# Kernel tuning notes

Measured on AMD Instinct MI355X. Metric: run time of the kernel, lower is better.

The kernel has to match this reference:

```python
import jax, jax.numpy as jnp
import numpy as np

D = 2048      # hidden
H = 16        # heads
HD = 128      # head dim
E = 64        # experts
K = 8         # top-k
F = 1024      # expert intermediate
B, S = 1, 256
EPS = 1e-05
THETA = 10000.0
SCALE = 0.08838834764831845  # 1/sqrt(128)


def _rms(x, w):
    return x * jax.lax.rsqrt(jnp.mean(x * x, axis=-1, keepdims=True) + EPS) * w


def _rotate_half(x):
    h = x.shape[-1] // 2
    return jnp.concatenate([-x[..., h:], x[..., :h]], axis=-1)


def setup_inputs() -> dict:
    key = jax.random.key(0)
    ks = jax.random.split(key, 16)
    std = 0.02
    return {
        "x": jax.random.normal(ks[0], (B, S, D), jnp.float32),
        "ln1_w": jnp.ones((D,), jnp.float32),
        "q_w": jax.random.normal(ks[1], (D, D), jnp.float32) * std,
        "k_w": jax.random.normal(ks[2], (D, D), jnp.float32) * std,
        "v_w": jax.random.normal(ks[3], (D, D), jnp.float32) * std,
        "o_w": jax.random.normal(ks[4], (D, D), jnp.float32) * std,
        "qn_w": jnp.ones((D,), jnp.float32),
        "kn_w": jnp.ones((D,), jnp.float32),
        "ln2_w": jnp.ones((D,), jnp.float32),
        "router_w": jax.random.normal(ks[5], (E, D), jnp.float32) * std,
        "gate_w": jax.random.normal(ks[6], (E, F, D), jnp.float32) * std,
        "up_w": jax.random.normal(ks[7], (E, F, D), jnp.float32) * std,
        "down_w": jax.random.normal(ks[8], (E, D, F), jnp.float32) * std,
    }


def reference(x, ln1_w, q_w, k_w, v_w, o_w, qn_w, kn_w, ln2_w,
              router_w, gate_w, up_w, down_w):
    b, s, d = x.shape
    # ---- attention ----
    xn = _rms(x, ln1_w)
    q = _rms(jnp.einsum('bsd,od->bso', xn, q_w), qn_w)
    k = _rms(jnp.einsum('bsd,od->bso', xn, k_w), kn_w)
    v = jnp.einsum('bsd,od->bso', xn, v_w)
    q = q.reshape(b, s, H, HD).transpose(0, 2, 1, 3)  # [b,h,s,hd]
    k = k.reshape(b, s, H, HD).transpose(0, 2, 1, 3)
    v = v.reshape(b, s, H, HD).transpose(0, 2, 1, 3)
    # RoPE
    inv_freq = 1.0 / (THETA ** (jnp.arange(0, HD, 2, dtype=jnp.float32) / HD))
    ang = jnp.arange(s, dtype=jnp.float32)[:, None] * inv_freq[None, :]  # [s, hd/2]
    emb = jnp.concatenate([ang, ang], axis=-1)
    cos, sin = jnp.cos(emb).astype(x.dtype), jnp.sin(emb).astype(x.dtype)
    q = q * cos + _rotate_half(q) * sin
    k = k * cos + _rotate_half(k) * sin
    scores = jnp.einsum('bhqd,bhkd->bhqk', q, k) * SCALE
    causal = jnp.tril(jnp.ones((s, s), bool))
    scores = jnp.where(causal, scores, jnp.finfo(scores.dtype).min)
    attn = jax.nn.softmax(scores, axis=-1)
    ctx = jnp.einsum('bhqk,bhkd->bhqd', attn, v)
    ctx = ctx.transpose(0, 2, 1, 3).reshape(b, s, d)
    h = x + jnp.einsum('bsd,od->bso', ctx, o_w)
    # ---- MoE ----
    hn = _rms(h, ln2_w)
    logits = jnp.einsum('bsd,ed->bse', hn, router_w)
    probs = jax.nn.softmax(logits.astype(jnp.float32), axis=-1)
    vals, idx = jax.lax.top_k(probs, K)  # [b,s,K]
    # dense combine weights [b,s,E]; OLMoE does not renormalize top-k probs
    combine = jnp.sum(jax.nn.one_hot(idx, E, dtype=jnp.float32) * vals[..., None], axis=-2)
    combine = combine.reshape(-1, E).astype(x.dtype)  # [T,E]
    xf = hn.reshape(-1, d)                            # [T,D]
    g = jnp.einsum('td,efd->etf', xf, gate_w)         # [E,T,F]
    u = jnp.einsum('td,efd->etf', xf, up_w)
    mid = jax.nn.silu(g) * u
    eo = jnp.einsum('etf,edf->etd', mid, down_w)      # [E,T,D]
    y = jnp.einsum('te,etd->td', combine, eo).reshape(b, s, d)
    return h + y
```

## Files before the change

### kernel.cpp

```cpp
#include <hip/hip_runtime.h>
#include <math.h>

#define DHID 2048
#define TOK 256
#define NHEAD 16
#define HDIM 128
#define NEXP 64
#define KSEL 8
#define FFD 1024
#define RMSEPS 1e-5f
#define ATTNSCALE 0.08838834764831845f

typedef short bf16x8 __attribute__((ext_vector_type(8)));
typedef float f32x4 __attribute__((ext_vector_type(4)));

__device__ __forceinline__ float bf2f(unsigned short u){
  union { unsigned int u; float f; } c; c.u = ((unsigned int)u)<<16; return c.f;
}
__device__ __forceinline__ unsigned short f2bf(float f){
  union { float f; unsigned int u; } c; c.f = f;
  unsigned int u = c.u + 0x7fffu + ((c.u>>16)&1u);
  return (unsigned short)(u>>16);
}
__device__ __forceinline__ unsigned int pk2(float a, float b){
  return (unsigned int)f2bf(a) | ((unsigned int)f2bf(b)<<16);
}

__global__ __launch_bounds__(256) void rms_kernel(const float* __restrict__ x,
    const float* __restrict__ w, unsigned short* __restrict__ obf,
    float* __restrict__ of32)
{
  int row = blockIdx.x, tid = threadIdx.x;
  const float* xr = x + (size_t)row*DHID;
  float4 a = *(const float4*)(xr + tid*8);
  float4 b = *(const float4*)(xr + tid*8 + 4);
  float ss = a.x*a.x+a.y*a.y+a.z*a.z+a.w*a.w + b.x*b.x+b.y*b.y+b.z*b.z+b.w*b.w;
  #pragma unroll
  for(int o=32;o>0;o>>=1) ss += __shfl_down(ss,o);
  __shared__ float red[4];
  if((tid&63)==0) red[tid>>6]=ss;
  __syncthreads();
  float r = rsqrtf((red[0]+red[1]+red[2]+red[3])*(1.0f/DHID) + RMSEPS);
  float v[8] = {a.x,a.y,a.z,a.w,b.x,b.y,b.z,b.w};
  unsigned short ob[8];
  #pragma unroll
  for(int j=0;j<8;j++){
    float val = v[j]*r*w[tid*8+j];
    ob[j]=f2bf(val);
    if(of32) of32[(size_t)row*DHID + tid*8 + j] = val;
  }
  uint4 o4;
  o4.x = (unsigned int)ob[0] | ((unsigned int)ob[1]<<16);
  o4.y = (unsigned int)ob[2] | ((unsigned int)ob[3]<<16);
  o4.z = (unsigned int)ob[4] | ((unsigned int)ob[5]<<16);
  o4.w = (unsigned int)ob[6] | ((unsigned int)ob[7]<<16);
  *(uint4*)(obf + (size_t)row*DHID + tid*8) = o4;
}

__global__ void rope_table_kernel(float* __restrict__ cs, float* __restrict__ sn){
  int i = blockIdx.x*256 + threadIdx.x;
  int s = i>>6, j = i&63;
  float invf = powf(10000.0f, -(float)j*(1.0f/64.0f));
  float ang = (float)s * invf;
  cs[i] = cosf(ang); sn[i] = sinf(ang);
}

__global__ __launch_bounds__(256) void gemm_qkv_kernel(
    const unsigned short* __restrict__ A,
    const float* __restrict__ qw, const float* __restrict__ kw, const float* __restrict__ vw,
    float* __restrict__ qo, float* __restrict__ ko, float* __restrict__ vo)
{
  int nt = blockIdx.x, mt = blockIdx.y;
  int which = nt>>5, nb = nt&31;
  const float* W = (which==0)? qw : (which==1)? kw : vw;
  float* OUT = (which==0)? qo : (which==1)? ko : vo;
  int n0 = nb*64, m0 = mt*64;
  __shared__ unsigned short As[64*64];
  __shared__ unsigned short Bs[64*64];
  int tid = threadIdx.x;
  int wid = tid>>6, lane = tid&63;
  int wm = wid>>1, wn = wid&1;
  int lr = lane&15, lg = lane>>4;
  int sr = tid>>2, sq = tid&3;
  f32x4 acc[2][2] = {};
  const unsigned short* Ap = A + (size_t)(m0+sr)*DHID + sq*16;
  const float* Bp = W + (size_t)(n0+sr)*DHID + sq*16;
  for(int k0=0;k0<DHID;k0+=64){
    uint4 a0 = *(const uint4*)(Ap + k0);
    uint4 a1 = *(const uint4*)(Ap + k0 + 8);
    float4 b0 = *(const float4*)(Bp + k0);
    float4 b1 = *(const float4*)(Bp + k0 + 4);
    float4 b2 = *(const float4*)(Bp + k0 + 8);
    float4 b3 = *(const float4*)(Bp + k0 + 12);
    int x7 = sr&7;
    *(uint4*)&As[sr*64 + (((sq*2)  ^ x7)*8)] = a0;
    *(uint4*)&As[sr*64 + (((sq*2+1)^ x7)*8)] = a1;
    uint4 p0 = make_uint4(pk2(b0.x,b0.y),pk2(b0.z,b0.w),pk2(b1.x,b1.y),pk2(b1.z,b1.w));
    uint4 p1 = make_uint4(pk2(b2.x,b2.y),pk2(b2.z,b2.w),pk2(b3.x,b3.y),pk2(b3.z,b3.w));
    *(uint4*)&Bs[sr*64 + (((sq*2)  ^ x7)*8)] = p0;
    *(uint4*)&Bs[sr*64 + (((sq*2+1)^ x7)*8)] = p1;
    __syncthreads();
    #pragma unroll
    for(int ki=0;ki<2;ki++){
      bf16x8 af[2], bfr[2];
      #pragma unroll
      for(int mi=0;mi<2;mi++){
        int r = wm*32 + mi*16 + lr;
        af[mi] = *(const bf16x8*)&As[r*64 + (((ki*4+lg)^(r&7))*8)];
      }
      #pragma unroll
      for(int ni=0;ni<2;ni++){
        int r = wn*32 + ni*16 + lr;
        bfr[ni] = *(const bf16x8*)&Bs[r*64 + (((ki*4+lg)^(r&7))*8)];
      }
      #pragma unroll
      for(int mi=0;mi<2;mi++)
        #pragma unroll
        for(int ni=0;ni<2;ni++)
          acc[mi][ni] = __builtin_amdgcn_mfma_f32_16x16x32_bf16(af[mi], bfr[ni], acc[mi][ni], 0,0,0);
    }
    __syncthreads();
  }
  #pragma unroll
  for(int mi=0;mi<2;mi++){
    #pragma unroll
    for(int ni=0;ni<2;ni++){
      int col = n0 + wn*32 + ni*16 + lr;
      int rowb = m0 + wm*32 + mi*16 + lg*4;
      #pragma unroll
      for(int rg=0;rg<4;rg++)
        OUT[(size_t)(rowb+rg)*DHID + col] = acc[mi][ni][rg];
    }
  }
}

__global__ __launch_bounds__(256) void gemm_o_kernel(const float* __restrict__ A,
  const float* __restrict__ W, const float* __restrict__ X,
  float* __restrict__ H, float* __restrict__ O)
{
  int nb = blockIdx.x, mt = blockIdx.y;
  int n0 = nb*64, m0 = mt*64;
  __shared__ unsigned short As[64*64];
  __shared__ unsigned short Bs[64*64];
  int tid = threadIdx.x;
  int wid = tid>>6, lane = tid&63;
  int wm = wid>>1, wn = wid&1;
  int lr = lane&15, lg = lane>>4;
  int sr = tid>>2, sq = tid&3;
  f32x4 acc[2][2] = {};
  const float* Ap = A + (size_t)(m0+sr)*DHID + sq*16;
  const float* Bp = W + (size_t)(n0+sr)*DHID + sq*16;
  for(int k0=0;k0<DHID;k0+=64){
    float4 a0=*(const float4*)(Ap+k0),   a1=*(const float4*)(Ap+k0+4);
    float4 a2=*(const float4*)(Ap+k0+8), a3=*(const float4*)(Ap+k0+12);
    float4 b0=*(const float4*)(Bp+k0),   b1=*(const float4*)(Bp+k0+4);
    float4 b2=*(const float4*)(Bp+k0+8), b3=*(const float4*)(Bp+k0+12);
    int x7 = sr&7;
    uint4 pa0 = make_uint4(pk2(a0.x,a0.y),pk2(a0.z,a0.w),pk2(a1.x,a1.y),pk2(a1.z,a1.w));
    uint4 pa1 = make_uint4(pk2(a2.x,a2.y),pk2(a2.z,a2.w),pk2(a3.x,a3.y),pk2(a3.z,a3.w));
    uint4 pb0 = make_uint4(pk2(b0.x,b0.y),pk2(b0.z,b0.w),pk2(b1.x,b1.y),pk2(b1.z,b1.w));
    uint4 pb1 = make_uint4(pk2(b2.x,b2.y),pk2(b2.z,b2.w),pk2(b3.x,b3.y),pk2(b3.z,b3.w));
    *(uint4*)&As[sr*64 + (((sq*2)  ^ x7)*8)] = pa0;
    *(uint4*)&As[sr*64 + (((sq*2+1)^ x7)*8)] = pa1;
    *(uint4*)&Bs[sr*64 + (((sq*2)  ^ x7)*8)] = pb0;
    *(uint4*)&Bs[sr*64 + (((sq*2+1)^ x7)*8)] = pb1;
    __syncthreads();
    #pragma unroll
    for(int ki=0;ki<2;ki++){
      bf16x8 af[2], bfr[2];
      #pragma unroll
      for(int mi=0;mi<2;mi++){
        int r = wm*32 + mi*16 + lr;
        af[mi] = *(const bf16x8*)&As[r*64 + (((ki*4+lg)^(r&7))*8)];
      }
      #pragma unroll
      for(int ni=0;ni<2;ni++){
        int r = wn*32 + ni*16 + lr;
        bfr[ni] = *(const bf16x8*)&Bs[r*64 + (((ki*4+lg)^(r&7))*8)];
      }
      #pragma unroll
      for(int mi=0;mi<2;mi++)
        #pragma unroll
        for(int ni=0;ni<2;ni++)
          acc[mi][ni] = __builtin_amdgcn_mfma_f32_16x16x32_bf16(af[mi], bfr[ni], acc[mi][ni], 0,0,0);
    }
    __syncthreads();
  }
  #pragma unroll
  for(int mi=0;mi<2;mi++){
    #pragma unroll
    for(int ni=0;ni<2;ni++){
      int col = n0 + wn*32 + ni*16 + lr;
      int rowb = m0 + wm*32 + mi*16 + lg*4;
      #pragma unroll
      for(int rg=0;rg<4;rg++){
        size_t idx = (size_t)(rowb+rg)*DHID + col;
        float v = acc[mi][ni][rg] + X[idx];
        H[idx] = v; O[idx] = v;
      }
    }
  }
}

__global__ __launch_bounds__(256) void qknorm_rope_kernel(const float* __restrict__ in,
   const float* __restrict__ w, const float* __restrict__ cs, const float* __restrict__ sn,
   float* __restrict__ out)
{
  int t = blockIdx.x, tid = threadIdx.x;
  __shared__ float xs[DHID];
  const float* xr = in + (size_t)t*DHID;
  float4 a = *(const float4*)(xr + tid*8);
  float4 b = *(const float4*)(xr + tid*8 + 4);
  *(float4*)&xs[tid*8] = a; *(float4*)&xs[tid*8+4] = b;
  float ss = a.x*a.x+a.y*a.y+a.z*a.z+a.w*a.w + b.x*b.x+b.y*b.y+b.z*b.z+b.w*b.w;
  #pragma unroll
  for(int o=32;o>0;o>>=1) ss += __shfl_down(ss,o);
  __shared__ float red[4];
  if((tid&63)==0) red[tid>>6]=ss;
  __syncthreads();
  float r = rsqrtf((red[0]+red[1]+red[2]+red[3])*(1.0f/DHID) + RMSEPS);
  int hh = tid>>4, jb = (tid&15)*4;
  #pragma unroll
  for(int p=0;p<4;p++){
    int j = jb+p;
    int i0 = hh*HDIM + j, i1 = i0+64;
    float va = xs[i0]*r*w[i0];
    float vb = xs[i1]*r*w[i1];
    float c = cs[t*64+j], s = sn[t*64+j];
    out[((size_t)(hh*TOK + t))*HDIM + j]    = va*c - vb*s;
    out[((size_t)(hh*TOK + t))*HDIM + j+64] = vb*c + va*s;
  }
}

__global__ __launch_bounds__(256) void vreshape_kernel(const float* __restrict__ v,
    float* __restrict__ vh)
{
  int t = blockIdx.x, tid = threadIdx.x;
  int i = tid*8;
  int hh = i>>7, d0 = i&127;
  float4 a = *(const float4*)(v + (size_t)t*DHID + i);
  float4 b = *(const float4*)(v + (size_t)t*DHID + i + 4);
  *(float4*)(vh + ((size_t)(hh*TOK+t))*HDIM + d0)     = a;
  *(float4*)(vh + ((size_t)(hh*TOK+t))*HDIM + d0 + 4) = b;
}

__global__ __launch_bounds__(256) void attn_kernel(const float* __restrict__ qh,
  const float* __restrict__ kh, const float* __restrict__ vh, float* __restrict__ ctx)
{
  int head = blockIdx.x>>4, qt = blockIdx.x&15;
  __shared__ float qs[16][132];
  __shared__ float sc[16][260];
  __shared__ float red[16][16];
  __shared__ float rmx[16], rsm[16];
  int tid = threadIdx.x;
  {
    int r = tid>>4, c = (tid&15)*8;
    const float* src = qh + ((size_t)(head*TOK + qt*16 + r))*HDIM + c;
    *(float4*)&qs[r][c]   = *(const float4*)(src);
    *(float4*)&qs[r][c+4] = *(const float4*)(src+4);
  }
  __syncthreads();
  int qi = tid&15, kk = tid>>4;
  int qg = qt*16 + qi;
  for(int k=kk; k<=qg; k+=16){
    const float* kp = kh + ((size_t)(head*TOK + k))*HDIM;
    float d = 0.f;
    #pragma unroll 8
    for(int c=0;c<128;c+=4){
      float4 kv = *(const float4*)(kp + c);
      float4 qv = *(const float4*)&qs[qi][c];
      d += qv.x*kv.x + qv.y*kv.y + qv.z*kv.z + qv.w*kv.w;
    }
    sc[qi][k] = d*ATTNSCALE;
  }
  float m = -1e30f;
  for(int k=kk;k<=qg;k+=16) m = fmaxf(m, sc[qi][k]);
  red[qi][kk] = m;
  __syncthreads();
  if(kk==0){
    float mm=-1e30f;
    #pragma unroll
    for(int j=0;j<16;j++) mm = fmaxf(mm, red[qi][j]);
    rmx[qi]=mm;
  }
  __syncthreads();
  float mm = rmx[qi];
  float s = 0.f;
  for(int k=kk;k<=qg;k+=16){ float pp = expf(sc[qi][k]-mm); sc[qi][k]=pp; s+=pp; }
  red[qi][kk]=s;
  __syncthreads();
  if(kk==0){
    float t_=0.f;
    #pragma unroll
    for(int j=0;j<16;j++) t_ += red[qi][j];
    rsm[qi]=t_;
  }
  __syncthreads();
  int dg = kk;
  float acc[8]={0,0,0,0,0,0,0,0};
  const float* vp = vh + (size_t)head*TOK*HDIM + dg*8;
  for(int k=0;k<=qg;k++){
    float p = sc[qi][k];
    float4 v0 = *(const float4*)(vp + (size_t)k*HDIM);
    float4 v1 = *(const float4*)(vp + (size_t)k*HDIM + 4);
    acc[0]+=p*v0.x; acc[1]+=p*v0.y; acc[2]+=p*v0.z; acc[3]+=p*v0.w;
    acc[4]+=p*v1.x; acc[5]+=p*v1.y; acc[6]+=p*v1.z; acc[7]+=p*v1.w;
  }
  float inv = 1.0f/rsm[qi];
  float* op = ctx + ((size_t)(qt*16+qi))*DHID + head*HDIM + dg*8;
  *(float4*)(op)   = make_float4(acc[0]*inv, acc[1]*inv, acc[2]*inv, acc[3]*inv);
  *(float4*)(op+4) = make_float4(acc[4]*inv, acc[5]*inv, acc[6]*inv, acc[7]*inv);
}

__global__ __launch_bounds__(256) void router_kernel(const float* __restrict__ hn,
    const float* __restrict__ rw, int* __restrict__ counts, int* __restrict__ toklist,
    float* __restrict__ wlist)
{
  int t = blockIdx.x, tid = threadIdx.x;
  __shared__ float xs[DHID];
  __shared__ float part[NEXP*4];
  __shared__ float probs[NEXP];
  *(float4*)&xs[tid*8]   = *(const float4*)(hn + (size_t)t*DHID + tid*8);
  *(float4*)&xs[tid*8+4] = *(const float4*)(hn + (size_t)t*DHID + tid*8+4);
  __syncthreads();
  int e = tid&63, c = tid>>6;
  const float* w = rw + (size_t)e*DHID + c*512;
  const float* xc = xs + c*512;
  float d = 0.f;
  for(int i=0;i<512;i+=4){
    float4 wv = *(const float4*)(w+i);
    d += xc[i]*wv.x + xc[i+1]*wv.y + xc[i+2]*wv.z + xc[i+3]*wv.w;
  }
  part[c*64 + e] = d;
  __syncthreads();
  if(tid<64){
    float logit = part[tid] + part[64+tid] + part[128+tid] + part[192+tid];
    float m = logit;
    #pragma unroll
    for(int o=32;o>0;o>>=1) m = fmaxf(m, __shfl_xor(m,o));
    float p = expf(logit - m);
    float s = p;
    #pragma unroll
    for(int o=32;o>0;o>>=1) s += __shfl_xor(s,o);
    probs[tid] = p/s;
  }
  __syncthreads();
  if(tid==0){
    unsigned long long used = 0ull;
    for(int r=0;r<KSEL;r++){
      float best = -1.f; int bi = 0;
      for(int j=0;j<NEXP;j++){
        if(!((used>>j)&1ull) && probs[j]>best){ best=probs[j]; bi=j; }
      }
      used |= (1ull<<bi);
      int slot = atomicAdd(&counts[bi],1);
      toklist[bi*TOK+slot] = t;
      wlist[bi*TOK+slot] = best;
    }
  }
}

__global__ void scan_kernel(const int* __restrict__ counts, int* __restrict__ offs){
  int e = threadIdx.x;
  int c = counts[e];
  int v = c;
  #pragma unroll
  for(int o=1;o<64;o<<=1){
    int n = __shfl_up(v,o);
    if(e>=o) v += n;
  }
  offs[e] = v - c;
}

__global__ __launch_bounds__(256) void moe_gateup_kernel(const unsigned short* __restrict__ hnb,
  const float* __restrict__ gw, const float* __restrict__ uw,
  const int* __restrict__ counts, const int* __restrict__ offs,
  const int* __restrict__ toklist, const float* __restrict__ wlist,
  unsigned short* __restrict__ mid)
{
  int fb = blockIdx.x, e = blockIdx.y, mc = blockIdx.z;
  int cnt = counts[e];
  if(mc*32 >= cnt) return;
  int base = offs[e];
  __shared__ unsigned short As[32*64];
  __shared__ unsigned short Bg[64*64];
  __shared__ unsigned short Bu[64*64];
  __shared__ int toks[32];
  __shared__ float cw[32];
  int tid = threadIdx.x;
  if(tid<32){
    int sl = mc*32 + tid;
    int cl = (sl<cnt)? sl : (cnt-1);
    toks[tid] = toklist[e*TOK + cl];
    cw[tid]   = (sl<cnt)? wlist[e*TOK+sl] : 0.0f;
  }
  __syncthreads();
  int wid=tid>>6, lane=tid&63, wm=wid>>1, wn=wid&1, lr=lane&15, lg=lane>>4;
  int arow=tid>>3, ac=tid&7;
  int sr=tid>>2, sq=tid&3;
  const unsigned short* Ap = hnb + (size_t)toks[arow]*DHID + ac*8;
  const float* Gp = gw + ((size_t)e*FFD + fb*64 + sr)*DHID + sq*16;
  const float* Up = uw + ((size_t)e*FFD + fb*64 + sr)*DHID + sq*16;
  f32x4 ag[2]={}, au[2]={};
  for(int k0=0;k0<DHID;k0+=64){
    uint4 av = *(const uint4*)(Ap + k0);
    float4 g0=*(const float4*)(Gp+k0),   g1=*(const float4*)(Gp+k0+4);
    float4 g2=*(const float4*)(Gp+k0+8), g3=*(const float4*)(Gp+k0+12);
    float4 u0=*(const float4*)(Up+k0),   u1=*(const float4*)(Up+k0+4);
    float4 u2=*(const float4*)(Up+k0+8), u3=*(const float4*)(Up+k0+12);
    int xa = arow&7, xb = sr&7;
    *(uint4*)&As[arow*64 + ((ac^xa)*8)] = av;
    uint4 pg0 = make_uint4(pk2(g0.x,g0.y),pk2(g0.z,g0.w),pk2(g1.x,g1.y),pk2(g1.z,g1.w));
    uint4 pg1 = make_uint4(pk2(g2.x,g2.y),pk2(g2.z,g2.w),pk2(g3.x,g3.y),pk2(g3.z,g3.w));
    uint4 pu0 = make_uint4(pk2(u0.x,u0.y),pk2(u0.z,u0.w),pk2(u1.x,u1.y),pk2(u1.z,u1.w));
    uint4 pu1 = make_uint4(pk2(u2.x,u2.y),pk2(u2.z,u2.w),pk2(u3.x,u3.y),pk2(u3.z,u3.w));
    *(uint4*)&Bg[sr*64 + (((sq*2)  ^ xb)*8)] = pg0;
    *(uint4*)&Bg[sr*64 + (((sq*2+1)^ xb)*8)] = pg1;
    *(uint4*)&Bu[sr*64 + (((sq*2)  ^ xb)*8)] = pu0;
    *(uint4*)&Bu[sr*64 + (((sq*2+1)^ xb)*8)] = pu1;
    __syncthreads();
    #pragma unroll
    for(int ki=0;ki<2;ki++){
      int ar = wm*16 + lr;
      bf16x8 af = *(const bf16x8*)&As[ar*64 + (((ki*4+lg)^(ar&7))*8)];
      #pragma unroll
      for(int ni=0;ni<2;ni++){
        int br = wn*32 + ni*16 + lr;
        int bo = br*64 + (((ki*4+lg)^(br&7))*8);
        bf16x8 bg = *(const bf16x8*)&Bg[bo];
        bf16x8 bu = *(const bf16x8*)&Bu[bo];
        ag[ni] = __builtin_amdgcn_mfma_f32_16x16x32_bf16(af,bg,ag[ni],0,0,0);
        au[ni] = __builtin_amdgcn_mfma_f32_16x16x32_bf16(af,bu,au[ni],0,0,0);
      }
    }
    __syncthreads();
  }
  #pragma unroll
  for(int ni=0;ni<2;ni++){
    int f = fb*64 + wn*32 + ni*16 + lr;
    #pragma unroll
    for(int rg=0;rg<4;rg++){
      int sl = wm*16 + lg*4 + rg;
      int slot = mc*32 + sl;
      if(slot < cnt){
        float g = ag[ni][rg], u = au[ni][rg];
        float mval = g/(1.0f+expf(-g))*u*cw[sl];
        mid[((size_t)(base+slot))*FFD + f] = f2bf(mval);
      }
    }
  }
}

__global__ __launch_bounds__(256) void moe_down_kernel(const unsigned short* __restrict__ mid,
  const float* __restrict__ dwn, const int* __restrict__ counts, const int* __restrict__ offs,
  const int* __restrict__ toklist, float* __restrict__ out)
{
  int nb=blockIdx.x, e=blockIdx.y, mc=blockIdx.z;
  int cnt=counts[e];
  if(mc*32>=cnt) return;
  int base=offs[e];
  __shared__ unsigned short As[32*64];
  __shared__ unsigned short Bs[64*64];
  __shared__ int toks[32];
  int tid=threadIdx.x;
  if(tid<32){ int sl=mc*32+tid; toks[tid]=toklist[e*TOK + ((sl<cnt)?sl:(cnt-1))]; }
  __syncthreads();
  int wid=tid>>6, lane=tid&63, wm=wid>>1, wn=wid&1, lr=lane&15, lg=lane>>4;
  int arow=tid>>3, ac=tid&7;
  int sr=tid>>2, sq=tid&3;
  int sla = mc*32+arow; if(sla>=cnt) sla=cnt-1;
  const unsigned short* Ap = mid + ((size_t)(base+sla))*FFD + ac*8;
  const float* Bp = dwn + ((size_t)e*DHID + nb*64 + sr)*FFD + sq*16;
  f32x4 acc[2]={};
  for(int k0=0;k0<FFD;k0+=64){
    uint4 av = *(const uint4*)(Ap+k0);
    float4 b0=*(const float4*)(Bp+k0),   b1=*(const float4*)(Bp+k0+4);
    float4 b2=*(const float4*)(Bp+k0+8), b3=*(const float4*)(Bp+k0+12);
    int xa=arow&7, xb=sr&7;
    *(uint4*)&As[arow*64+((ac^xa)*8)] = av;
    uint4 p0=make_uint4(pk2(b0.x,b0.y),pk2(b0.z,b0.w),pk2(b1.x,b1.y),pk2(b1.z,b1.w));
    uint4 p1=make_uint4(pk2(b2.x,b2.y),pk2(b2.z,b2.w),pk2(b3.x,b3.y),pk2(b3.z,b3.w));
    *(uint4*)&Bs[sr*64+(((sq*2)^xb)*8)] = p0;
    *(uint4*)&Bs[sr*64+(((sq*2+1)^xb)*8)] = p1;
    __syncthreads();
    #pragma unroll
    for(int ki=0;ki<2;ki++){
      int ar=wm*16+lr;
      bf16x8 af=*(const bf16x8*)&As[ar*64+(((ki*4+lg)^(ar&7))*8)];
      #pragma unroll
      for(int ni=0;ni<2;ni++){
        int br=wn*32+ni*16+lr;
        bf16x8 bb=*(const bf16x8*)&Bs[br*64+(((ki*4+lg)^(br&7))*8)];
        acc[ni]=__builtin_amdgcn_mfma_f32_16x16x32_bf16(af,bb,acc[ni],0,0,0);
      }
    }
    __syncthreads();
  }
  #pragma unroll
  for(int ni=0;ni<2;ni++){
    int d = nb*64 + wn*32 + ni*16 + lr;
    #pragma unroll
    for(int rg=0;rg<4;rg++){
      int sl=wm*16+lg*4+rg, slot=mc*32+sl;
      if(slot<cnt) atomicAdd(out + (size_t)toks[sl]*DHID + d, acc[ni][rg]);
    }
  }
}

extern "C" void kernel_launch(void* const* d_in, const int* in_sizes, int n_in,
                              void* d_out, int out_size, void* d_ws, size_t ws_size,
                              hipStream_t stream)
{
  (void)in_sizes; (void)n_in; (void)out_size; (void)ws_size;
  const float* x    = (const float*)d_in[0];
  const float* ln1w = (const float*)d_in[1];
  const float* qw   = (const float*)d_in[2];
  const float* kw   = (const float*)d_in[3];
  const float* vw   = (const float*)d_in[4];
  const float* ow   = (const float*)d_in[5];
  const float* qnw  = (const float*)d_in[6];
  const float* knw  = (const float*)d_in[7];
  const float* ln2w = (const float*)d_in[8];
  const float* rw   = (const float*)d_in[9];
  const float* gw   = (const float*)d_in[10];
  const float* uw   = (const float*)d_in[11];
  const float* dwn  = (const float*)d_in[12];
  float* out = (float*)d_out;

  char* p = (char*)d_ws;
  auto alloc = [&](size_t bytes)->void*{ void* r = (void*)p; p += (bytes + 255) & ~(size_t)255; return r; };
  unsigned short* xnb = (unsigned short*)alloc((size_t)TOK*DHID*2);
  float* qf   = (float*)alloc((size_t)TOK*DHID*4);
  float* kf   = (float*)alloc((size_t)TOK*DHID*4);
  float* vf   = (float*)alloc((size_t)TOK*DHID*4);
  float* qh   = (float*)alloc((size_t)TOK*DHID*4);
  float* kh   = (float*)alloc((size_t)TOK*DHID*4);
  float* vh   = (float*)alloc((size_t)TOK*DHID*4);
  float* ctx  = (float*)alloc((size_t)TOK*DHID*4);
  float* hbuf = (float*)alloc((size_t)TOK*DHID*4);
  float* hnf  = (float*)alloc((size_t)TOK*DHID*4);
  unsigned short* hnb = (unsigned short*)alloc((size_t)TOK*DHID*2);
  float* csb  = (float*)alloc((size_t)TOK*64*4);
  float* snb  = (float*)alloc((size_t)TOK*64*4);
  int* counts = (int*)alloc(NEXP*4);
  int* offs   = (int*)alloc(NEXP*4);
  int* toklist= (int*)alloc((size_t)NEXP*TOK*4);
  float* wlist= (float*)alloc((size_t)NEXP*TOK*4);
  unsigned short* mid = (unsigned short*)alloc((size_t)TOK*KSEL*FFD*2);

  rope_table_kernel<<<64,256,0,stream>>>(csb,snb);
  rms_kernel<<<TOK,256,0,stream>>>(x, ln1w, xnb, nullptr);
  gemm_qkv_kernel<<<dim3(96,4),256,0,stream>>>(xnb,qw,kw,vw,qf,kf,vf);
  qknorm_rope_kernel<<<TOK,256,0,stream>>>(qf,qnw,csb,snb,qh);
  qknorm_rope_kernel<<<TOK,256,0,stream>>>(kf,knw,csb,snb,kh);
  vreshape_kernel<<<TOK,256,0,stream>>>(vf,vh);
  attn_kernel<<<256,256,0,stream>>>(qh,kh,vh,ctx);
  gemm_o_kernel<<<dim3(32,4),256,0,stream>>>(ctx,ow,x,hbuf,out);
  rms_kernel<<<TOK,256,0,stream>>>(hbuf, ln2w, hnb, hnf);
  hipMemsetAsync(counts,0,NEXP*4,stream);
  router_kernel<<<TOK,256,0,stream>>>(hnf,rw,counts,toklist,wlist);
  scan_kernel<<<1,64,0,stream>>>(counts,offs);
  moe_gateup_kernel<<<dim3(16,NEXP,8),256,0,stream>>>(hnb,gw,uw,counts,offs,toklist,wlist,mid);
  moe_down_kernel<<<dim3(32,NEXP,8),256,0,stream>>>(mid,dwn,counts,offs,toklist,out);
}
```

Before: 680.7 us.

## Load MoE GEMM fragments directly to registers with register double-buffering

The MoE gate/up and down kernels stop staging A and B tiles through shared memory. Each lane now loads its MFMA fragment straight from global memory and converts fp32 weights to bf16 in registers. The next K-stage is prefetched into registers while the current MFMAs run, and the block barriers go away. The cost is more register pressure, and each lane now issues two separate 32-byte loads per row instead of one contiguous 64-byte chunk, which may hurt coalescing.

```diff
diff --git a/kernel.cpp b/kernel.cpp
--- a/kernel.cpp
+++ b/kernel.cpp
@@ -24,6 +24,14 @@
 }
 __device__ __forceinline__ unsigned int pk2(float a, float b){
   return (unsigned int)f2bf(a) | ((unsigned int)f2bf(b)<<16);
+}
+__device__ __forceinline__ bf16x8 pack8f(float4 a, float4 b){
+  union { uint4 u; bf16x8 v; } c;
+  c.u = make_uint4(pk2(a.x,a.y), pk2(a.z,a.w), pk2(b.x,b.y), pk2(b.z,b.w));
+  return c.v;
+}
+__device__ __forceinline__ bf16x8 as_bf8(uint4 u){
+  union { uint4 u; bf16x8 v; } c; c.u = u; return c.v;
 }
 
 __global__ __launch_bounds__(256) void rms_kernel(const float* __restrict__ x,
@@ -382,9 +390,6 @@
   int cnt = counts[e];
   if(mc*32 >= cnt) return;
   int base = offs[e];
-  __shared__ unsigned short As[32*64];
-  __shared__ unsigned short Bg[64*64];
-  __shared__ unsigned short Bu[64*64];
   __shared__ int toks[32];
   __shared__ float cw[32];
   int tid = threadIdx.x;
@@ -396,44 +401,52 @@
   }
   __syncthreads();
   int wid=tid>>6, lane=tid&63, wm=wid>>1, wn=wid&1, lr=lane&15, lg=lane>>4;
-  int arow=tid>>3, ac=tid&7;
-  int sr=tid>>2, sq=tid&3;
-  const unsigned short* Ap = hnb + (size_t)toks[arow]*DHID + ac*8;
-  const float* Gp = gw + ((size_t)e*FFD + fb*64 + sr)*DHID + sq*16;
-  const float* Up = uw + ((size_t)e*FFD + fb*64 + sr)*DHID + sq*16;
+  const unsigned short* Ap = hnb + (size_t)toks[wm*16+lr]*DHID + lg*8;
+  size_t gbase = ((size_t)e*FFD + fb*64 + wn*32 + lr)*DHID + lg*8;
+  const float* Gp = gw + gbase;
+  const float* Up = uw + gbase;
+
+  uint4  ar[2];
+  float4 gr[2][2][2], ur[2][2][2];
   f32x4 ag[2]={}, au[2]={};
+
+  auto load_stage = [&](int K0){
+    ar[0] = *(const uint4*)(Ap + K0);
+    ar[1] = *(const uint4*)(Ap + K0 + 32);
+    #pragma unroll
+    for(int ni=0;ni<2;ni++){
+      #pragma unroll
+      for(int ki=0;ki<2;ki++){
+        gr[ni][ki][0] = *(const float4*)(Gp + ni*16*DHID + K0 + ki*32);
+        gr[ni][ki][1] = *(const float4*)(Gp + ni*16*DHID + K0 + ki*32 + 4);
+        ur[ni][ki][0] = *(const float4*)(Up + ni*16*DHID + K0 + ki*32);
+        ur[ni][ki][1] = *(const float4*)(Up + ni*16*DHID + K0 + ki*32 + 4);
+      }
+    }
+  };
+
+  load_stage(0);
   for(int k0=0;k0<DHID;k0+=64){
-    uint4 av = *(const uint4*)(Ap + k0);
-    float4 g0=*(const float4*)(Gp+k0),   g1=*(const float4*)(Gp+k0+4);
-    float4 g2=*(const float4*)(Gp+k0+8), g3=*(const float4*)(Gp+k0+12);
-    float4 u0=*(const float4*)(Up+k0),   u1=*(const float4*)(Up+k0+4);
-    float4 u2=*(const float4*)(Up+k0+8), u3=*(const float4*)(Up+k0+12);
-    int xa = arow&7, xb = sr&7;
-    *(uint4*)&As[arow*64 + ((ac^xa)*8)] = av;
-    uint4 pg0 = make_uint4(pk2(g0.x,g0.y),pk2(g0.z,g0.w),pk2(g1.x,g1.y),pk2(g1.z,g1.w));
-    uint4 pg1 = make_uint4(pk2(g2.x,g2.y),pk2(g2.z,g2.w),pk2(g3.x,g3.y),pk2(g3.z,g3.w));
-    uint4 pu0 = make_uint4(pk2(u0.x,u0.y),pk2(u0.z,u0.w),pk2(u1.x,u1.y),pk2(u1.z,u1.w));
-    uint4 pu1 = make_uint4(pk2(u2.x,u2.y),pk2(u2.z,u2.w),pk2(u3.x,u3.y),pk2(u3.z,u3.w));
-    *(uint4*)&Bg[sr*64 + (((sq*2)  ^ xb)*8)] = pg0;
-    *(uint4*)&Bg[sr*64 + (((sq*2+1)^ xb)*8)] = pg1;
-    *(uint4*)&Bu[sr*64 + (((sq*2)  ^ xb)*8)] = pu0;
-    *(uint4*)&Bu[sr*64 + (((sq*2+1)^ xb)*8)] = pu1;
-    __syncthreads();
+    bf16x8 af[2], gf[2][2], uf[2][2];
+    #pragma unroll
+    for(int ki=0;ki<2;ki++) af[ki] = as_bf8(ar[ki]);
+    #pragma unroll
+    for(int ni=0;ni<2;ni++){
+      #pragma unroll
+      for(int ki=0;ki<2;ki++){
+        gf[ni][ki] = pack8f(gr[ni][ki][0], gr[ni][ki][1]);
+        uf[ni][ki] = pack8f(ur[ni][ki][0], ur[ni][ki][1]);
+      }
+    }
+    if(k0+64<DHID) load_stage(k0+64);
     #pragma unroll
     for(int ki=0;ki<2;ki++){
-      int ar = wm*16 + lr;
-      bf16x8 af = *(const bf16x8*)&As[ar*64 + (((ki*4+lg)^(ar&7))*8)];
       #pragma unroll
       for(int ni=0;ni<2;ni++){
-        int br = wn*32 + ni*16 + lr;
-        int bo = br*64 + (((ki*4+lg)^(br&7))*8);
-        bf16x8 bg = *(const bf16x8*)&Bg[bo];
-        bf16x8 bu = *(const bf16x8*)&Bu[bo];
-        ag[ni] = __builtin_amdgcn_mfma_f32_16x16x32_bf16(af,bg,ag[ni],0,0,0);
-        au[ni] = __builtin_amdgcn_mfma_f32_16x16x32_bf16(af,bu,au[ni],0,0,0);
-      }
-    }
-    __syncthreads();
+        ag[ni] = __builtin_amdgcn_mfma_f32_16x16x32_bf16(af[ki], gf[ni][ki], ag[ni], 0,0,0);
+        au[ni] = __builtin_amdgcn_mfma_f32_16x16x32_bf16(af[ki], uf[ni][ki], au[ni], 0,0,0);
+      }
+    }
   }
   #pragma unroll
   for(int ni=0;ni<2;ni++){
@@ -459,42 +472,51 @@
   int cnt=counts[e];
   if(mc*32>=cnt) return;
   int base=offs[e];
-  __shared__ unsigned short As[32*64];
-  __shared__ unsigned short Bs[64*64];
   __shared__ int toks[32];
   int tid=threadIdx.x;
   if(tid<32){ int sl=mc*32+tid; toks[tid]=toklist[e*TOK + ((sl<cnt)?sl:(cnt-1))]; }
   __syncthreads();
   int wid=tid>>6, lane=tid&63, wm=wid>>1, wn=wid&1, lr=lane&15, lg=lane>>4;
-  int arow=tid>>3, ac=tid&7;
-  int sr=tid>>2, sq=tid&3;
-  int sla = mc*32+arow; if(sla>=cnt) sla=cnt-1;
-  const unsigned short* Ap = mid + ((size_t)(base+sla))*FFD + ac*8;
-  const float* Bp = dwn + ((size_t)e*DHID + nb*64 + sr)*FFD + sq*16;
+  int slot0 = mc*32 + wm*16 + lr;
+  int sla = (slot0<cnt)? slot0 : (cnt-1);
+  const unsigned short* Ap = mid + (size_t)(base+sla)*FFD + lg*8;
+  const float* Bp = dwn + ((size_t)e*DHID + nb*64 + wn*32 + lr)*FFD + lg*8;
+
+  uint4  ar[2];
+  float4 dr[2][2][2];
   f32x4 acc[2]={};
+
+  auto load_stage = [&](int K0){
+    ar[0] = *(const uint4*)(Ap + K0);
+    ar[1] = *(const uint4*)(Ap + K0 + 32);
+    #pragma unroll
+    for(int ni=0;ni<2;ni++){
+      #pragma unroll
+      for(int ki=0;ki<2;ki++){
+        dr[ni][ki][0] = *(const float4*)(Bp + ni*16*FFD + K0 + ki*32);
+        dr[ni][ki][1] = *(const float4*)(Bp + ni*16*FFD + K0 + ki*32 + 4);
+      }
+    }
+  };
+
+  load_stage(0);
   for(int k0=0;k0<FFD;k0+=64){
-    uint4 av = *(const uint4*)(Ap+k0);
-    float4 b0=*(const float4*)(Bp+k0),   b1=*(const float4*)(Bp+k0+4);
-    float4 b2=*(const float4*)(Bp+k0+8), b3=*(const float4*)(Bp+k0+12);
-    int xa=arow&7, xb=sr&7;
-    *(uint4*)&As[arow*64+((ac^xa)*8)] = av;
-    uint4 p0=make_uint4(pk2(b0.x,b0.y),pk2(b0.z,b0.w),pk2(b1.x,b1.y),pk2(b1.z,b1.w));
-    uint4 p1=make_uint4(pk2(b2.x,b2.y),pk2(b2.z,b2.w),pk2(b3.x,b3.y),pk2(b3.z,b3.w));
-    *(uint4*)&Bs[sr*64+(((sq*2)^xb)*8)] = p0;
-    *(uint4*)&Bs[sr*64+(((sq*2+1)^xb)*8)] = p1;
-    __syncthreads();
+    bf16x8 af[2], df[2][2];
+    #pragma unroll
+    for(int ki=0;ki<2;ki++) af[ki] = as_bf8(ar[ki]);
+    #pragma unroll
+    for(int ni=0;ni<2;ni++){
+      #pragma unroll
+      for(int ki=0;ki<2;ki++)
+        df[ni][ki] = pack8f(dr[ni][ki][0], dr[ni][ki][1]);
+    }
+    if(k0+64<FFD) load_stage(k0+64);
     #pragma unroll
     for(int ki=0;ki<2;ki++){
-      int ar=wm*16+lr;
-      bf16x8 af=*(const bf16x8*)&As[ar*64+(((ki*4+lg)^(ar&7))*8)];
-      #pragma unroll
-      for(int ni=0;ni<2;ni++){
-        int br=wn*32+ni*16+lr;
-        bf16x8 bb=*(const bf16x8*)&Bs[br*64+(((ki*4+lg)^(br&7))*8)];
-        acc[ni]=__builtin_amdgcn_mfma_f32_16x16x32_bf16(af,bb,acc[ni],0,0,0);
-      }
-    }
-    __syncthreads();
+      #pragma unroll
+      for(int ni=0;ni<2;ni++)
+        acc[ni] = __builtin_amdgcn_mfma_f32_16x16x32_bf16(af[ki], df[ni][ki], acc[ni], 0,0,0);
+    }
   }
   #pragma unroll
   for(int ni=0;ni<2;ni++){
```

Result: slower. 888.8 us (+30.6%).
